# Kernel tuning notes

Hardware: AMD Instinct MI355X
Metric: run time of the kernel (lower is better)

The kernel has to match this reference:

```python
import jax, jax.numpy as jnp
import numpy as np

EPS = 1e-5

def ste_sign(x):
    # straight-through sign: forward = sign(x), backward = identity (BNN STE)
    return x + jax.lax.stop_gradient(jnp.sign(x) - x)

def conv(x, w, b, stride, pad):
    y = jax.lax.conv_general_dilated(x, w, (stride, stride), [(pad, pad), (pad, pad)],
                                     dimension_numbers=('NCHW', 'OIHW', 'NCHW'))
    return y + b[None, :, None, None]

def maxpool3s2(x):
    return jax.lax.reduce_window(x, -jnp.inf, jax.lax.max, (1, 1, 3, 3), (1, 1, 2, 2), 'VALID')

def bn2d(x, g, c, m, v):
    return g[None, :, None, None] * (x - m[None, :, None, None]) * jax.lax.rsqrt(v[None, :, None, None] + EPS) + c[None, :, None, None]

def bn1d(x, g, c, m, v):
    return g * (x - m) * jax.lax.rsqrt(v + EPS) + c

def ht(x):
    return jnp.clip(x, -1.0, 1.0)

def _bn_params(k, C):
    k1, k2, k3, k4 = jax.random.split(k, 4)
    g = 1.0 + 0.05 * jax.random.normal(k1, (C,), dtype=jnp.float32)
    c = 0.05 * jax.random.normal(k2, (C,), dtype=jnp.float32)
    m = 0.05 * jax.random.normal(k3, (C,), dtype=jnp.float32)
    v = 0.5 + jax.random.uniform(k4, (C,), dtype=jnp.float32)
    return g, c, m, v

def setup_inputs() -> dict:
    key = jax.random.key(0)
    ks = jax.random.split(key, 20)
    rn = lambda k, s: (0.05 * jax.random.normal(k, s)).astype(jnp.float32)
    d = {}
    d['x'] = jax.random.normal(ks[0], (128, 3, 224, 224), dtype=jnp.float32)
    conv_shapes = [(96, 3, 11, 11), (256, 96, 5, 5), (384, 256, 3, 3), (384, 384, 3, 3), (256, 384, 3, 3)]
    bn_chs = [96, 256, 384, 384, 256]
    for i, (cs, C) in enumerate(zip(conv_shapes, bn_chs), start=1):
        kw, kb, kbn = jax.random.split(ks[i], 3)
        d[f'W{i}'] = rn(kw, cs)
        d[f'b{i}'] = rn(kb, (cs[0],))
        g, c, m, v = _bn_params(kbn, C)
        d[f'g{i}'], d[f'c{i}'], d[f'm{i}'], d[f'v{i}'] = g, c, m, v
    fc_shapes = [(4096, 256 * 6 * 6), (4096, 4096), (1000, 4096)]
    for j, fs in enumerate(fc_shapes, start=6):
        kw, kb, kbn = jax.random.split(ks[j], 3)
        d[f'W{j}'] = rn(kw, fs)
        d[f'b{j}'] = rn(kb, (fs[0],))
        g, c, m, v = _bn_params(kbn, fs[0])
        d[f'g{j}'], d[f'c{j}'], d[f'm{j}'], d[f'v{j}'] = g, c, m, v
    return d

def reference(x,
              W1, b1, g1, c1, m1, v1,
              W2, b2, g2, c2, m2, v2,
              W3, b3, g3, c3, m3, v3,
              W4, b4, g4, c4, m4, v4,
              W5, b5, g5, c5, m5, v5,
              W6, b6, g6, c6, m6, v6,
              W7, b7, g7, c7, m7, v7,
              W8, b8, g8, c8, m8, v8):
    # features0: first conv keeps float input (C==3 is not binarized), binary weights
    h = conv(x, ste_sign(W1), b1, 4, 2)          # [B,96,55,55]
    h = ste_sign(h)                               # explicit torch.sign(x) in forward
    h = ht(bn2d(maxpool3s2(h), g1, c1, m1, v1))   # [B,96,27,27]
    h = conv(ste_sign(h), ste_sign(W2), b2, 1, 2) # [B,256,27,27]
    h = ht(bn2d(maxpool3s2(h), g2, c2, m2, v2))   # [B,256,13,13]
    h = conv(ste_sign(h), ste_sign(W3), b3, 1, 1)
    h = ht(bn2d(h, g3, c3, m3, v3))               # [B,384,13,13]
    h = conv(ste_sign(h), ste_sign(W4), b4, 1, 1)
    h = ht(bn2d(h, g4, c4, m4, v4))               # [B,384,13,13]
    h = conv(ste_sign(h), ste_sign(W5), b5, 1, 1)
    h = ht(bn2d(maxpool3s2(h), g5, c5, m5, v5))   # [B,256,6,6]
    h = h.reshape(h.shape[0], 256 * 6 * 6)
    h = ht(bn1d(ste_sign(h) @ ste_sign(W6).T + b6, g6, c6, m6, v6))  # [B,4096]
    h = ht(bn1d(ste_sign(h) @ ste_sign(W7).T + b7, g7, c7, m7, v7))  # [B,4096]
    h = bn1d(ste_sign(h) @ ste_sign(W8).T + b8, g8, c8, m8, v8)      # [B,1000]
    return jax.nn.log_softmax(h, axis=-1)
```

## Files before the change

### kernel.cpp

```cpp
#include <hip/hip_runtime.h>
#include <hip/hip_bf16.h>
#include <math.h>

#define EPSV 1e-5f
typedef unsigned long long u64;

__device__ __forceinline__ int isgn(float x) { return (x > 0.f) - (x < 0.f); }
__device__ __forceinline__ float bnf(float x, float g, float c, float m, float v) {
    return g * (x - m) * rsqrtf(v + EPSV) + c;
}


__global__ __launch_bounds__(256) void pad_x(const float* __restrict__ x,
                                             float* __restrict__ Xp) {
    int idx = blockIdx.x * 256 + threadIdx.x;
    const int total = 128 * 3 * 228 * 228;
    if (idx >= total) return;
    int iwp = idx % 228;
    int t = idx / 228;
    int ihp = t % 228;
    int nc = t / 228;
    int iw = iwp - 2, ih = ihp - 2;
    float v = 0.f;
    if ((unsigned)iw < 224u && (unsigned)ih < 224u)
        v = x[((size_t)nc * 224 + ih) * 224 + iw];
    Xp[idx] = v;
}

__global__ __launch_bounds__(256) void pack_w1t(const float* __restrict__ W,
                                                float* __restrict__ Wp) {
    int idx = blockIdx.x * 256 + threadIdx.x;
    const int total = 6 * 3 * 11 * 11 * 16;
    if (idx >= total) return;
    int j = idx % 16;
    int t = idx / 16;
    int kw = t % 11; t /= 11;
    int kh = t % 11; t /= 11;
    int ci = t % 3;
    int cog = t / 3;
    int co = cog * 16 + j;
    float w = W[(((size_t)co * 3 + ci) * 11 + kh) * 11 + kw];
    Wp[idx] = (w > 0.f) ? 1.f : -1.f;
}

__global__ __launch_bounds__(256) void conv1_tile(
    const float* __restrict__ Xp, const float* __restrict__ Wp,
    const float* __restrict__ bias, signed char* __restrict__ S1) {
    const int Hp = 228, Wpad = 228, OH = 55, OW = 55;
    int n = blockIdx.x, ohg = blockIdx.y, cog = blockIdx.z;
    int lane = threadIdx.x & 63;
    int oh = ohg * 4 + (threadIdx.x >> 6);
    bool act = (lane < OW) && (oh < OH);
    int owc = min(lane, OW - 1);
    int ohc = min(oh, OH - 1);

    float acc[16];
    #pragma unroll
    for (int j = 0; j < 16; ++j) acc[j] = 0.f;

    const float* __restrict__ wbase = Wp + (size_t)cog * (3 * 11 * 11 * 16);

    for (int ci = 0; ci < 3; ++ci) {
        const float* xrow0 = Xp + ((size_t)(n * 3 + ci) * Hp + ohc * 4) * Wpad + owc * 4;
        const float* __restrict__ wci = wbase + ci * (11 * 11 * 16);
        for (int kh = 0; kh < 11; ++kh) {
            const float4* xr = (const float4*)(xrow0 + kh * Wpad);
            float4 a = xr[0], b = xr[1], c = xr[2];
            float xv[12] = {a.x, a.y, a.z, a.w, b.x, b.y, b.z, b.w, c.x, c.y, c.z, c.w};
            const float* __restrict__ wk = wci + kh * (11 * 16);
            #pragma unroll
            for (int kw = 0; kw < 11; ++kw) {
                #pragma unroll
                for (int j = 0; j < 16; ++j)
                    acc[j] += wk[kw * 16 + j] * xv[kw];
            }
        }
    }

    if (act) {
        size_t base = ((size_t)(n * 96 + cog * 16) * OH + oh) * OW + lane;
        #pragma unroll
        for (int j = 0; j < 16; ++j) {
            float a = acc[j] + bias[cog * 16 + j];
            S1[base + (size_t)j * (OH * OW)] = (signed char)isgn(a);
        }
    }
}


template <int K, int CW>
__global__ __launch_bounds__(256) void pack_wc(const float* __restrict__ W,
                                               u64* __restrict__ out, int Ci, int Co) {
    int wid = blockIdx.x * 4 + (threadIdx.x >> 6);
    int b = threadIdx.x & 63;
    int total = Co * K * K * CW;
    if (wid >= total) return;
    int cw = wid % CW;
    int t = wid / CW;
    int kw = t % K; t /= K;
    int kh = t % K;
    int co = t / K;
    int ci = cw * 64 + b;
    int bit = 0;
    if (ci < Ci) bit = W[(((size_t)co * Ci + ci) * K + kh) * K + kw] > 0.f;
    u64 mask = __ballot(bit);
    if (b == 0) out[wid] = mask;
}

__global__ __launch_bounds__(256) void pack_wfc6(const float* __restrict__ W,
                                                 u64* __restrict__ out) {
    int wid = blockIdx.x * 4 + (threadIdx.x >> 6);
    int b = threadIdx.x & 63;
    int o = wid / 144;
    int j = wid % 144;
    int c = (j & 3) * 64 + b;
    int p = j >> 2;
    float val = W[(size_t)o * 9216 + c * 36 + p];
    u64 mask = __ballot(val > 0.f);
    if (b == 0) out[(size_t)j * 4096 + o] = mask;
}

__global__ __launch_bounds__(256) void pack_wfc(const float* __restrict__ W,
                                                u64* __restrict__ out, int O) {
    int wid = blockIdx.x * 4 + (threadIdx.x >> 6);
    int b = threadIdx.x & 63;
    if (wid >= O * 64) return;
    int o = wid >> 6;
    int j = wid & 63;
    float val = W[(size_t)o * 4096 + j * 64 + b];
    u64 mask = __ballot(val > 0.f);
    if (b == 0) out[(size_t)j * O + o] = mask;
}

__global__ __launch_bounds__(128) void pool1_pack(
    const signed char* __restrict__ in,
    const float* __restrict__ g, const float* __restrict__ cb,
    const float* __restrict__ m, const float* __restrict__ v,
    u64* __restrict__ out) {
    const int C = 96, H = 55, W = 55, OW = 27, OH = 27;
    int bx = blockIdx.x;
    int ow = bx % OW;
    int t = bx / OW;
    int oh = t % OH;
    int n = t / OH;
    int c = threadIdx.x;
    int bit = 0;
    if (c < C) {
        const signed char* ip = in + ((size_t)(n * C + c) * H + oh * 2) * W + ow * 2;
        int mx = -127;
        #pragma unroll
        for (int kh = 0; kh < 3; ++kh)
            #pragma unroll
            for (int kw = 0; kw < 3; ++kw)
                mx = max(mx, (int)ip[kh * W + kw]);
        float y = bnf((float)mx, g[c], cb[c], m[c], v[c]);
        bit = y > 0.f;
    }
    u64 mask = __ballot(bit);
    if ((threadIdx.x & 63) == 0) out[(size_t)bx * 2 + (threadIdx.x >> 6)] = mask;
}

__global__ __launch_bounds__(256) void pool_pack_f32(
    const float* __restrict__ in,
    const float* __restrict__ g, const float* __restrict__ cb,
    const float* __restrict__ m, const float* __restrict__ v,
    u64* __restrict__ out, int C, int H, int W, int OH, int OW) {
    int bx = blockIdx.x;
    int ow = bx % OW;
    int t = bx / OW;
    int oh = t % OH;
    int n = t / OH;
    int c = threadIdx.x;
    const float* ip = in + ((size_t)(n * C + c) * H + oh * 2) * W + ow * 2;
    float mx = -INFINITY;
    #pragma unroll
    for (int kh = 0; kh < 3; ++kh)
        #pragma unroll
        for (int kw = 0; kw < 3; ++kw)
            mx = fmaxf(mx, ip[kh * W + kw]);
    float y = bnf(mx, g[c], cb[c], m[c], v[c]);
    u64 mask = __ballot(y > 0.f);
    if ((c & 63) == 0) out[(size_t)bx * (C >> 6) + (c >> 6)] = mask;
}

__global__ __launch_bounds__(384) void bn_pack_f32(
    const float* __restrict__ in,
    const float* __restrict__ g, const float* __restrict__ cb,
    const float* __restrict__ m, const float* __restrict__ v,
    u64* __restrict__ out, int C, int HW) {
    int bx = blockIdx.x;
    int p = bx % HW;
    int n = bx / HW;
    int c = threadIdx.x;
    float val = in[((size_t)n * C + c) * HW + p];
    float y = bnf(val, g[c], cb[c], m[c], v[c]);
    u64 mask = __ballot(y > 0.f);
    if ((c & 63) == 0) out[(size_t)bx * (C >> 6) + (c >> 6)] = mask;
}

__global__ __launch_bounds__(256) void bn_pack_fc(
    const float* __restrict__ in,
    const float* __restrict__ g, const float* __restrict__ cb,
    const float* __restrict__ m, const float* __restrict__ v,
    u64* __restrict__ out) {
    int c = blockIdx.x * 256 + threadIdx.x;
    int n = blockIdx.y;
    float val = in[(size_t)n * 4096 + c];
    float y = bnf(val, g[c], cb[c], m[c], v[c]);
    u64 mask = __ballot(y > 0.f);
    if ((threadIdx.x & 63) == 0) out[(size_t)n * 64 + (c >> 6)] = mask;
}

template <int K, int P, int CW>
__global__ __launch_bounds__(256) void bconv_bit(
    const u64* __restrict__ act, const u64* __restrict__ wgt,
    const float* __restrict__ bias, float* __restrict__ out,
    int N, int Ci, int Co, int H, int W) {
    int p = blockIdx.x * 256 + threadIdx.x;
    if (p >= N * H * W) return;
    int ow = p % W;
    int t = p / W;
    int oh = t % H;
    int n = t / H;
    int co = blockIdx.y;
    const u64* wrow = wgt + (size_t)co * K * K * CW;
    int mism = 0, nval = 0;
    #pragma unroll
    for (int kh = 0; kh < K; ++kh) {
        int ih = oh - P + kh;
        if ((unsigned)ih >= (unsigned)H) continue;
        #pragma unroll
        for (int kw = 0; kw < K; ++kw) {
            int iw = ow - P + kw;
            if ((unsigned)iw >= (unsigned)W) continue;
            const u64* ap = act + ((size_t)(n * H + ih) * W + iw) * CW;
            const u64* wp = wrow + (kh * K + kw) * CW;
            #pragma unroll
            for (int cw = 0; cw < CW; ++cw)
                mism += __popcll(ap[cw] ^ wp[cw]);
            nval++;
        }
    }
    float acc = (float)(nval * Ci - 2 * mism) + bias[co];
    out[((size_t)(n * Co + co) * H + oh) * W + ow] = acc;
}

__global__ __launch_bounds__(256) void fc_bit(
    const u64* __restrict__ actw, const u64* __restrict__ wgtT,
    const float* __restrict__ bias, float* __restrict__ out, int IW, int O) {
    int o = blockIdx.x * 256 + threadIdx.x;
    if (o >= O) return;
    int n0 = blockIdx.y * 8;
    const u64* ap = actw + (size_t)n0 * IW;
    int acc[8];
    #pragma unroll
    for (int r = 0; r < 8; ++r) acc[r] = 0;
    for (int w = 0; w < IW; ++w) {
        u64 wv = wgtT[(size_t)w * O + o];
        #pragma unroll
        for (int r = 0; r < 8; ++r)
            acc[r] += __popcll(ap[(size_t)r * IW + w] ^ wv);
    }
    float b = bias[o];
    #pragma unroll
    for (int r = 0; r < 8; ++r)
        out[(size_t)(n0 + r) * O + o] = (float)(IW * 64 - 2 * acc[r]) + b;
}

__global__ __launch_bounds__(256) void bn_lsm_kernel(
    const float* __restrict__ in,
    const float* __restrict__ g, const float* __restrict__ cb,
    const float* __restrict__ m, const float* __restrict__ v,
    float* __restrict__ out, int O) {
    int n = blockIdx.x;
    __shared__ float buf[1000];
    __shared__ float red[256];
    int tid = threadIdx.x;
    float lmax = -INFINITY;
    for (int o = tid; o < O; o += 256) {
        float y = bnf(in[(size_t)n * O + o], g[o], cb[o], m[o], v[o]);
        buf[o] = y;
        lmax = fmaxf(lmax, y);
    }
    red[tid] = lmax;
    __syncthreads();
    for (int s = 128; s > 0; s >>= 1) {
        if (tid < s) red[tid] = fmaxf(red[tid], red[tid + s]);
        __syncthreads();
    }
    float mx = red[0];
    __syncthreads();
    float lsum = 0.f;
    for (int o = tid; o < O; o += 256) lsum += expf(buf[o] - mx);
    red[tid] = lsum;
    __syncthreads();
    for (int s = 128; s > 0; s >>= 1) {
        if (tid < s) red[tid] += red[tid + s];
        __syncthreads();
    }
    float lse = mx + logf(red[0]);
    for (int o = tid; o < O; o += 256) out[(size_t)n * O + o] = buf[o] - lse;
}

extern "C" void kernel_launch(void* const* d_in, const int* in_sizes, int n_in,
                              void* d_out, int out_size, void* d_ws, size_t ws_size,
                              hipStream_t stream) {
    const float* x = (const float*)d_in[0];
    auto L = [&](int layer, int k) -> const float* {
        return (const float*)d_in[1 + (layer - 1) * 6 + k];
    };

    char* ws = (char*)d_ws;
    float* A        = (float*)(ws + 0);
    float* Xp       = A;
    signed char* S1 = (signed char*)(ws + 95551488);
    u64* P1  = (u64*)(ws + 132722688);
    u64* P2  = (u64*)(ws + 134215680);
    u64* P3a = (u64*)(ws + 134907904);
    u64* P3b = (u64*)(ws + 135946240);
    u64* P5  = (u64*)(ws + 136984576);
    u64* F7  = (u64*)(ws + 137132032);
    u64* F8  = (u64*)(ws + 137197568);
    u64* Wc2 = (u64*)(ws + 137263104);
    u64* Wc3 = (u64*)(ws + 137365504);
    u64* Wc4 = (u64*)(ws + 137476096);
    u64* Wc5 = (u64*)(ws + 137641984);
    u64* Wf6 = (u64*)(ws + 137752576);
    u64* Wf7 = (u64*)(ws + 142471168);
    u64* Wf8 = (u64*)(ws + 144568320);
    float* Wp1 = (float*)(ws + 145080320);

    pack_w1t<<<137, 256, 0, stream>>>(L(1, 0), Wp1);
    pad_x<<<(128 * 3 * 228 * 228 + 255) / 256, 256, 0, stream>>>(x, Xp);
    pack_wc<5, 2><<<3200, 256, 0, stream>>>(L(2, 0), Wc2, 96, 256);
    pack_wc<3, 4><<<3456, 256, 0, stream>>>(L(3, 0), Wc3, 256, 384);
    pack_wc<3, 6><<<5184, 256, 0, stream>>>(L(4, 0), Wc4, 384, 384);
    pack_wc<3, 6><<<3456, 256, 0, stream>>>(L(5, 0), Wc5, 384, 256);
    pack_wfc6<<<147456, 256, 0, stream>>>(L(6, 0), Wf6);
    pack_wfc<<<65536, 256, 0, stream>>>(L(7, 0), Wf7, 4096);
    pack_wfc<<<16000, 256, 0, stream>>>(L(8, 0), Wf8, 1000);

    {
        dim3 g(128, 14, 6);
        conv1_tile<<<g, 256, 0, stream>>>(Xp, Wp1, L(1, 1), S1);
    }
    pool1_pack<<<93312, 128, 0, stream>>>(S1, L(1, 2), L(1, 3), L(1, 4), L(1, 5), P1);
    {
        dim3 g((128 * 27 * 27 + 255) / 256, 256);
        bconv_bit<5, 2, 2><<<g, 256, 0, stream>>>(P1, Wc2, L(2, 1), A, 128, 96, 256, 27, 27);
    }
    pool_pack_f32<<<128 * 13 * 13, 256, 0, stream>>>(A, L(2, 2), L(2, 3), L(2, 4), L(2, 5),
                                                     P2, 256, 27, 27, 13, 13);
    {
        dim3 g((128 * 13 * 13 + 255) / 256, 384);
        bconv_bit<3, 1, 4><<<g, 256, 0, stream>>>(P2, Wc3, L(3, 1), A, 128, 256, 384, 13, 13);
    }
    bn_pack_f32<<<128 * 169, 384, 0, stream>>>(A, L(3, 2), L(3, 3), L(3, 4), L(3, 5),
                                               P3a, 384, 169);
    {
        dim3 g((128 * 13 * 13 + 255) / 256, 384);
        bconv_bit<3, 1, 6><<<g, 256, 0, stream>>>(P3a, Wc4, L(4, 1), A, 128, 384, 384, 13, 13);
    }
    bn_pack_f32<<<128 * 169, 384, 0, stream>>>(A, L(4, 2), L(4, 3), L(4, 4), L(4, 5),
                                               P3b, 384, 169);
    {
        dim3 g((128 * 13 * 13 + 255) / 256, 256);
        bconv_bit<3, 1, 6><<<g, 256, 0, stream>>>(P3b, Wc5, L(5, 1), A, 128, 384, 256, 13, 13);
    }
    pool_pack_f32<<<128 * 6 * 6, 256, 0, stream>>>(A, L(5, 2), L(5, 3), L(5, 4), L(5, 5),
                                                   P5, 256, 13, 13, 6, 6);
    {
        dim3 g(16, 16);
        fc_bit<<<g, 256, 0, stream>>>(P5, Wf6, L(6, 1), A, 144, 4096);
    }
    {
        dim3 g(16, 128);
        bn_pack_fc<<<g, 256, 0, stream>>>(A, L(6, 2), L(6, 3), L(6, 4), L(6, 5), F7);
    }
    {
        dim3 g(16, 16);
        fc_bit<<<g, 256, 0, stream>>>(F7, Wf7, L(7, 1), A, 64, 4096);
    }
    {
        dim3 g(16, 128);
        bn_pack_fc<<<g, 256, 0, stream>>>(A, L(7, 2), L(7, 3), L(7, 4), L(7, 5), F8);
    }
    {
        dim3 g(4, 16);
        fc_bit<<<g, 256, 0, stream>>>(F8, Wf8, L(8, 1), A, 64, 1000);
    }
    bn_lsm_kernel<<<128, 256, 0, stream>>>(A, L(8, 2), L(8, 3), L(8, 4), L(8, 5),
                                           (float*)d_out, 1000);
}
```

Before: 1.944 ms.

## Switch binary conv pipeline to NHWC with per-thread output channels and bit-packed pool1

Conv1 now writes 16-channel sign bitmasks in NHWC order instead of int8 NCHW, and pool1 becomes a bitwise OR-max followed by a precomputed BN sign lookup. The bit-convs are replaced by a kernel where each thread owns one output channel, keeps its packed weights in registers, and loops over a few pixels that share the same activation words. Outputs go to NHWC so the pool/BN pack kernels read channel-contiguous data. The FC6 weight packing is also staged through LDS for coalesced reads. Keeping many weight words in registers raises register pressure, and each block now covers far fewer pixels.

```diff
diff --git a/kernel.cpp b/kernel.cpp
--- a/kernel.cpp
+++ b/kernel.cpp
@@ -4,8 +4,8 @@
 
 #define EPSV 1e-5f
 typedef unsigned long long u64;
-
-__device__ __forceinline__ int isgn(float x) { return (x > 0.f) - (x < 0.f); }
+typedef unsigned short u16;
+
 __device__ __forceinline__ float bnf(float x, float g, float c, float m, float v) {
     return g * (x - m) * rsqrtf(v + EPSV) + c;
 }
@@ -45,7 +45,7 @@
 
 __global__ __launch_bounds__(256) void conv1_tile(
     const float* __restrict__ Xp, const float* __restrict__ Wp,
-    const float* __restrict__ bias, signed char* __restrict__ S1) {
+    const float* __restrict__ bias, u16* __restrict__ S1b) {
     const int Hp = 228, Wpad = 228, OH = 55, OW = 55;
     int n = blockIdx.x, ohg = blockIdx.y, cog = blockIdx.z;
     int lane = threadIdx.x & 63;
@@ -78,19 +78,50 @@
     }
 
     if (act) {
-        size_t base = ((size_t)(n * 96 + cog * 16) * OH + oh) * OW + lane;
+        unsigned mask = 0;
+        #pragma unroll
+        for (int j = 0; j < 16; ++j)
+            mask |= (acc[j] + bias[cog * 16 + j] > 0.f) ? (1u << j) : 0u;
+        S1b[((size_t)(n * OH + oh) * OW + lane) * 8 + cog] = (u16)mask;
+    }
+}
+
+__global__ __launch_bounds__(256) void pool1_bit(
+    const u16* __restrict__ S1b,
+    const float* __restrict__ g, const float* __restrict__ cb,
+    const float* __restrict__ m, const float* __restrict__ v,
+    u16* __restrict__ P1) {
+    int n = blockIdx.x / 27;
+    int ohp = blockIdx.x % 27;
+    int tid = threadIdx.x;
+    if (tid >= 216) return;
+    int cog = tid & 7;
+    int owp = tid >> 3;
+    unsigned res = 0;
+    if (cog < 6) {
+        unsigned tp = 0, tn = 0;
         #pragma unroll
         for (int j = 0; j < 16; ++j) {
-            float a = acc[j] + bias[cog * 16 + j];
-            S1[base + (size_t)j * (OH * OW)] = (signed char)isgn(a);
+            int c = cog * 16 + j;
+            float gg = g[c], cc = cb[c], mm = m[c], vv = v[c];
+            tp |= (bnf(1.f, gg, cc, mm, vv) > 0.f) ? (1u << j) : 0u;
+            tn |= (bnf(-1.f, gg, cc, mm, vv) > 0.f) ? (1u << j) : 0u;
         }
-    }
+        unsigned mk = 0;
+        #pragma unroll
+        for (int kh = 0; kh < 3; ++kh)
+            #pragma unroll
+            for (int kw = 0; kw < 3; ++kw)
+                mk |= S1b[((size_t)(n * 55 + 2 * ohp + kh) * 55 + 2 * owp + kw) * 8 + cog];
+        res = (mk & tp) | (~mk & tn & 0xffffu);
+    }
+    P1[((size_t)(n * 27 + ohp) * 27 + owp) * 8 + cog] = (u16)res;
 }
 
 
 template <int K, int CW>
-__global__ __launch_bounds__(256) void pack_wc(const float* __restrict__ W,
-                                               u64* __restrict__ out, int Ci, int Co) {
+__global__ __launch_bounds__(256) void pack_wc_t(const float* __restrict__ W,
+                                                 u64* __restrict__ out, int Ci, int Co) {
     int wid = blockIdx.x * 4 + (threadIdx.x >> 6);
     int b = threadIdx.x & 63;
     int total = Co * K * K * CW;
@@ -104,20 +135,26 @@
     int bit = 0;
     if (ci < Ci) bit = W[(((size_t)co * Ci + ci) * K + kh) * K + kw] > 0.f;
     u64 mask = __ballot(bit);
-    if (b == 0) out[wid] = mask;
-}
-
-__global__ __launch_bounds__(256) void pack_wfc6(const float* __restrict__ W,
-                                                 u64* __restrict__ out) {
-    int wid = blockIdx.x * 4 + (threadIdx.x >> 6);
-    int b = threadIdx.x & 63;
-    int o = wid / 144;
-    int j = wid % 144;
-    int c = (j & 3) * 64 + b;
-    int p = j >> 2;
-    float val = W[(size_t)o * 9216 + c * 36 + p];
-    u64 mask = __ballot(val > 0.f);
-    if (b == 0) out[(size_t)j * 4096 + o] = mask;
+    if (b == 0) out[(size_t)(((kh * K + kw) * CW + cw)) * Co + co] = mask;
+}
+
+__global__ __launch_bounds__(256) void pack_wfc6_t(const float* __restrict__ W,
+                                                   u64* __restrict__ out) {
+    __shared__ float lds[256 * 37];
+    int o = blockIdx.x;
+    int tid = threadIdx.x;
+    for (int i = tid; i < 9216; i += 256) {
+        int c = i / 36, p = i - c * 36;
+        lds[c * 37 + p] = W[(size_t)o * 9216 + i];
+    }
+    __syncthreads();
+    int wave = tid >> 6, lane = tid & 63;
+    for (int jj = wave; jj < 144; jj += 4) {
+        int p = jj >> 2, cw = jj & 3;
+        int bit = lds[(cw * 64 + lane) * 37 + p] > 0.f;
+        u64 mask = __ballot(bit);
+        if (lane == 0) out[(size_t)jj * 4096 + o] = mask;
+    }
 }
 
 __global__ __launch_bounds__(256) void pack_wfc(const float* __restrict__ W,
@@ -132,35 +169,44 @@
     if (b == 0) out[(size_t)j * O + o] = mask;
 }
 
-__global__ __launch_bounds__(128) void pool1_pack(
-    const signed char* __restrict__ in,
-    const float* __restrict__ g, const float* __restrict__ cb,
-    const float* __restrict__ m, const float* __restrict__ v,
-    u64* __restrict__ out) {
-    const int C = 96, H = 55, W = 55, OW = 27, OH = 27;
-    int bx = blockIdx.x;
-    int ow = bx % OW;
-    int t = bx / OW;
-    int oh = t % OH;
-    int n = t / OH;
-    int c = threadIdx.x;
-    int bit = 0;
-    if (c < C) {
-        const signed char* ip = in + ((size_t)(n * C + c) * H + oh * 2) * W + ow * 2;
-        int mx = -127;
-        #pragma unroll
-        for (int kh = 0; kh < 3; ++kh)
+template <int K, int P, int CW, int HW, int W, int CO, int PIX, int CI>
+__global__ __launch_bounds__(CO) void bconv_co(
+    const u64* __restrict__ act, const u64* __restrict__ wT,
+    const float* __restrict__ bias, float* __restrict__ out) {
+    const int H = HW / W;
+    int co = threadIdx.x;
+    int n = blockIdx.y;
+    int p0 = blockIdx.x * PIX;
+    u64 wreg[K * K * CW];
+    #pragma unroll
+    for (int t = 0; t < K * K * CW; ++t) wreg[t] = wT[(size_t)t * CO + co];
+    float b = bias[co];
+    #pragma unroll
+    for (int p = 0; p < PIX; ++p) {
+        int pix = p0 + p;
+        if (pix >= HW) break;
+        int oh = pix / W, ow = pix - oh * W;
+        int mism = 0, nval = 0;
+        #pragma unroll
+        for (int kh = 0; kh < K; ++kh) {
+            int ih = oh - P + kh;
+            if ((unsigned)ih >= (unsigned)H) continue;
             #pragma unroll
-            for (int kw = 0; kw < 3; ++kw)
-                mx = max(mx, (int)ip[kh * W + kw]);
-        float y = bnf((float)mx, g[c], cb[c], m[c], v[c]);
-        bit = y > 0.f;
-    }
-    u64 mask = __ballot(bit);
-    if ((threadIdx.x & 63) == 0) out[(size_t)bx * 2 + (threadIdx.x >> 6)] = mask;
-}
-
-__global__ __launch_bounds__(256) void pool_pack_f32(
+            for (int kw = 0; kw < K; ++kw) {
+                int iw = ow - P + kw;
+                if ((unsigned)iw >= (unsigned)W) continue;
+                const u64* ap = act + ((size_t)(n * H + ih) * W + iw) * CW;
+                #pragma unroll
+                for (int cw = 0; cw < CW; ++cw)
+                    mism += __popcll(ap[cw] ^ wreg[(kh * K + kw) * CW + cw]);
+                nval++;
+            }
+        }
+        out[((size_t)n * HW + pix) * CO + co] = (float)(nval * CI - 2 * mism) + b;
+    }
+}
+
+__global__ __launch_bounds__(256) void pool_pack_nhwc(
     const float* __restrict__ in,
     const float* __restrict__ g, const float* __restrict__ cb,
     const float* __restrict__ m, const float* __restrict__ v,
@@ -171,28 +217,25 @@
     int oh = t % OH;
     int n = t / OH;
     int c = threadIdx.x;
-    const float* ip = in + ((size_t)(n * C + c) * H + oh * 2) * W + ow * 2;
     float mx = -INFINITY;
     #pragma unroll
     for (int kh = 0; kh < 3; ++kh)
         #pragma unroll
         for (int kw = 0; kw < 3; ++kw)
-            mx = fmaxf(mx, ip[kh * W + kw]);
+            mx = fmaxf(mx, in[((size_t)(n * H + oh * 2 + kh) * W + ow * 2 + kw) * C + c]);
     float y = bnf(mx, g[c], cb[c], m[c], v[c]);
     u64 mask = __ballot(y > 0.f);
     if ((c & 63) == 0) out[(size_t)bx * (C >> 6) + (c >> 6)] = mask;
 }
 
-__global__ __launch_bounds__(384) void bn_pack_f32(
+__global__ __launch_bounds__(384) void bn_pack_nhwc(
     const float* __restrict__ in,
     const float* __restrict__ g, const float* __restrict__ cb,
     const float* __restrict__ m, const float* __restrict__ v,
-    u64* __restrict__ out, int C, int HW) {
+    u64* __restrict__ out, int C) {
     int bx = blockIdx.x;
-    int p = bx % HW;
-    int n = bx / HW;
     int c = threadIdx.x;
-    float val = in[((size_t)n * C + c) * HW + p];
+    float val = in[(size_t)bx * C + c];
     float y = bnf(val, g[c], cb[c], m[c], v[c]);
     u64 mask = __ballot(y > 0.f);
     if ((c & 63) == 0) out[(size_t)bx * (C >> 6) + (c >> 6)] = mask;
@@ -209,40 +252,6 @@
     float y = bnf(val, g[c], cb[c], m[c], v[c]);
     u64 mask = __ballot(y > 0.f);
     if ((threadIdx.x & 63) == 0) out[(size_t)n * 64 + (c >> 6)] = mask;
-}
-
-template <int K, int P, int CW>
-__global__ __launch_bounds__(256) void bconv_bit(
-    const u64* __restrict__ act, const u64* __restrict__ wgt,
-    const float* __restrict__ bias, float* __restrict__ out,
-    int N, int Ci, int Co, int H, int W) {
-    int p = blockIdx.x * 256 + threadIdx.x;
-    if (p >= N * H * W) return;
-    int ow = p % W;
-    int t = p / W;
-    int oh = t % H;
-    int n = t / H;
-    int co = blockIdx.y;
-    const u64* wrow = wgt + (size_t)co * K * K * CW;
-    int mism = 0, nval = 0;
-    #pragma unroll
-    for (int kh = 0; kh < K; ++kh) {
-        int ih = oh - P + kh;
-        if ((unsigned)ih >= (unsigned)H) continue;
-        #pragma unroll
-        for (int kw = 0; kw < K; ++kw) {
-            int iw = ow - P + kw;
-            if ((unsigned)iw >= (unsigned)W) continue;
-            const u64* ap = act + ((size_t)(n * H + ih) * W + iw) * CW;
-            const u64* wp = wrow + (kh * K + kw) * CW;
-            #pragma unroll
-            for (int cw = 0; cw < CW; ++cw)
-                mism += __popcll(ap[cw] ^ wp[cw]);
-            nval++;
-        }
-    }
-    float acc = (float)(nval * Ci - 2 * mism) + bias[co];
-    out[((size_t)(n * Co + co) * H + oh) * W + ow] = acc;
 }
 
 __global__ __launch_bounds__(256) void fc_bit(
@@ -311,64 +320,63 @@
     };
 
     char* ws = (char*)d_ws;
-    float* A        = (float*)(ws + 0);
-    float* Xp       = A;
-    signed char* S1 = (signed char*)(ws + 95551488);
-    u64* P1  = (u64*)(ws + 132722688);
-    u64* P2  = (u64*)(ws + 134215680);
-    u64* P3a = (u64*)(ws + 134907904);
-    u64* P3b = (u64*)(ws + 135946240);
-    u64* P5  = (u64*)(ws + 136984576);
-    u64* F7  = (u64*)(ws + 137132032);
-    u64* F8  = (u64*)(ws + 137197568);
-    u64* Wc2 = (u64*)(ws + 137263104);
-    u64* Wc3 = (u64*)(ws + 137365504);
-    u64* Wc4 = (u64*)(ws + 137476096);
-    u64* Wc5 = (u64*)(ws + 137641984);
-    u64* Wf6 = (u64*)(ws + 137752576);
-    u64* Wf7 = (u64*)(ws + 142471168);
-    u64* Wf8 = (u64*)(ws + 144568320);
-    float* Wp1 = (float*)(ws + 145080320);
+    float* A   = (float*)(ws + 0);
+    float* Xp  = A;
+    u16* S1b   = (u16*)(ws + 95551488);
+    u16* P1u   = (u16*)(ws + 101746688);
+    u64* P1    = (u64*)P1u;
+    u64* P2    = (u64*)(ws + 103239680);
+    u64* P3a   = (u64*)(ws + 103931904);
+    u64* P3b   = (u64*)(ws + 104970240);
+    u64* P5    = (u64*)(ws + 106008576);
+    u64* F7    = (u64*)(ws + 106156032);
+    u64* F8    = (u64*)(ws + 106221568);
+    u64* WcT2  = (u64*)(ws + 106287104);
+    u64* WcT3  = (u64*)(ws + 106389504);
+    u64* WcT4  = (u64*)(ws + 106500096);
+    u64* WcT5  = (u64*)(ws + 106665984);
+    u64* Wf6   = (u64*)(ws + 106776576);
+    u64* Wf7   = (u64*)(ws + 111495168);
+    u64* Wf8   = (u64*)(ws + 113592320);
+    float* Wp1 = (float*)(ws + 114104320);
 
     pack_w1t<<<137, 256, 0, stream>>>(L(1, 0), Wp1);
     pad_x<<<(128 * 3 * 228 * 228 + 255) / 256, 256, 0, stream>>>(x, Xp);
-    pack_wc<5, 2><<<3200, 256, 0, stream>>>(L(2, 0), Wc2, 96, 256);
-    pack_wc<3, 4><<<3456, 256, 0, stream>>>(L(3, 0), Wc3, 256, 384);
-    pack_wc<3, 6><<<5184, 256, 0, stream>>>(L(4, 0), Wc4, 384, 384);
-    pack_wc<3, 6><<<3456, 256, 0, stream>>>(L(5, 0), Wc5, 384, 256);
-    pack_wfc6<<<147456, 256, 0, stream>>>(L(6, 0), Wf6);
+    pack_wc_t<5, 2><<<3200, 256, 0, stream>>>(L(2, 0), WcT2, 96, 256);
+    pack_wc_t<3, 4><<<3456, 256, 0, stream>>>(L(3, 0), WcT3, 256, 384);
+    pack_wc_t<3, 6><<<5184, 256, 0, stream>>>(L(4, 0), WcT4, 384, 384);
+    pack_wc_t<3, 6><<<3456, 256, 0, stream>>>(L(5, 0), WcT5, 384, 256);
+    pack_wfc6_t<<<4096, 256, 0, stream>>>(L(6, 0), Wf6);
     pack_wfc<<<65536, 256, 0, stream>>>(L(7, 0), Wf7, 4096);
     pack_wfc<<<16000, 256, 0, stream>>>(L(8, 0), Wf8, 1000);
 
     {
         dim3 g(128, 14, 6);
-        conv1_tile<<<g, 256, 0, stream>>>(Xp, Wp1, L(1, 1), S1);
-    }
-    pool1_pack<<<93312, 128, 0, stream>>>(S1, L(1, 2), L(1, 3), L(1, 4), L(1, 5), P1);
-    {
-        dim3 g((128 * 27 * 27 + 255) / 256, 256);
-        bconv_bit<5, 2, 2><<<g, 256, 0, stream>>>(P1, Wc2, L(2, 1), A, 128, 96, 256, 27, 27);
-    }
-    pool_pack_f32<<<128 * 13 * 13, 256, 0, stream>>>(A, L(2, 2), L(2, 3), L(2, 4), L(2, 5),
-                                                     P2, 256, 27, 27, 13, 13);
-    {
-        dim3 g((128 * 13 * 13 + 255) / 256, 384);
-        bconv_bit<3, 1, 4><<<g, 256, 0, stream>>>(P2, Wc3, L(3, 1), A, 128, 256, 384, 13, 13);
-    }
-    bn_pack_f32<<<128 * 169, 384, 0, stream>>>(A, L(3, 2), L(3, 3), L(3, 4), L(3, 5),
-                                               P3a, 384, 169);
-    {
-        dim3 g((128 * 13 * 13 + 255) / 256, 384);
-        bconv_bit<3, 1, 6><<<g, 256, 0, stream>>>(P3a, Wc4, L(4, 1), A, 128, 384, 384, 13, 13);
-    }
-    bn_pack_f32<<<128 * 169, 384, 0, stream>>>(A, L(4, 2), L(4, 3), L(4, 4), L(4, 5),
-                                               P3b, 384, 169);
-    {
-        dim3 g((128 * 13 * 13 + 255) / 256, 256);
-        bconv_bit<3, 1, 6><<<g, 256, 0, stream>>>(P3b, Wc5, L(5, 1), A, 128, 384, 256, 13, 13);
-    }
-    pool_pack_f32<<<128 * 6 * 6, 256, 0, stream>>>(A, L(5, 2), L(5, 3), L(5, 4), L(5, 5),
-                                                   P5, 256, 13, 13, 6, 6);
+        conv1_tile<<<g, 256, 0, stream>>>(Xp, Wp1, L(1, 1), S1b);
+    }
+    pool1_bit<<<128 * 27, 256, 0, stream>>>(S1b, L(1, 2), L(1, 3), L(1, 4), L(1, 5), P1u);
+    {
+        dim3 g((729 + 7) / 8, 128);
+        bconv_co<5, 2, 2, 729, 27, 256, 8, 96><<<g, 256, 0, stream>>>(P1, WcT2, L(2, 1), A);
+    }
+    pool_pack_nhwc<<<128 * 13 * 13, 256, 0, stream>>>(A, L(2, 2), L(2, 3), L(2, 4), L(2, 5),
+                                                      P2, 256, 27, 27, 13, 13);
+    {
+        dim3 g((169 + 3) / 4, 128);
+        bconv_co<3, 1, 4, 169, 13, 384, 4, 256><<<g, 384, 0, stream>>>(P2, WcT3, L(3, 1), A);
+    }
+    bn_pack_nhwc<<<128 * 169, 384, 0, stream>>>(A, L(3, 2), L(3, 3), L(3, 4), L(3, 5), P3a, 384);
+    {
+        dim3 g((169 + 3) / 4, 128);
+        bconv_co<3, 1, 6, 169, 13, 384, 4, 384><<<g, 384, 0, stream>>>(P3a, WcT4, L(4, 1), A);
+    }
+    bn_pack_nhwc<<<128 * 169, 384, 0, stream>>>(A, L(4, 2), L(4, 3), L(4, 4), L(4, 5), P3b, 384);
+    {
+        dim3 g((169 + 3) / 4, 128);
+        bconv_co<3, 1, 6, 169, 13, 256, 4, 384><<<g, 256, 0, stream>>>(P3b, WcT5, L(5, 1), A);
+    }
+    pool_pack_nhwc<<<128 * 6 * 6, 256, 0, stream>>>(A, L(5, 2), L(5, 3), L(5, 4), L(5, 5),
+                                                    P5, 256, 13, 13, 6, 6);
     {
         dim3 g(16, 16);
         fc_bit<<<g, 256, 0, stream>>>(P5, Wf6, L(6, 1), A, 144, 4096);
```

After: 1.749 ms. 1.11x faster.
